# Kernel optimization log

Measured on AMD Instinct MI355X. Metric: run time of the kernel, lower is better.

## Reference

```python
import jax, jax.numpy as jnp
import numpy as np

EPSILON = 1e-05


def setup_inputs() -> dict:
    key = jax.random.key(0)
    k1, k2, k3 = jax.random.split(key, 3)
    B, T, D, K = 8, 4096, 256, 2048
    hidden_states = jax.random.normal(k1, (B, T, D), dtype=jnp.float32)
    embed_sum = jax.random.normal(k2, (K, D), dtype=jnp.float32)
    # cluster usage counts are positive in practice
    cluster_usage = jax.random.uniform(k3, (K,), dtype=jnp.float32) * 10.0 + 0.1
    return {
        "hidden_states": hidden_states,
        "embed_sum": embed_sum,
        "cluster_usage": cluster_usage,
    }


def reference(hidden_states, embed_sum, cluster_usage):
    # embed = embed_sum / clamp(cluster_usage, eps)   -> [K, D]
    embed = embed_sum / jnp.clip(cluster_usage, EPSILON, None)[:, None]

    shape = hidden_states.shape
    x = hidden_states.reshape(-1, shape[-1])  # [N, D]

    # squared L2 distances via norm expansion (argmin equals argmin of cdist p=2)
    x_sq = jnp.sum(x * x, axis=-1, keepdims=True)          # [N, 1]
    e_sq = jnp.sum(embed * embed, axis=-1)[None, :]         # [1, K]
    dots = jnp.einsum("nd,kd->nk", x, embed)               # [N, K]
    dists = x_sq - 2.0 * dots + e_sq                        # [N, K]

    embed_ind = jnp.argmin(dists, axis=-1)                 # [N]
    embed_ind = embed_ind.reshape(shape[:-1])              # [B, T]

    # decode: embedding lookup
    quantize = embed[embed_ind]                             # [B, T, D]
    return quantize, embed_ind
```

## Files before the change

kernel.cpp:

```cpp
#include <hip/hip_runtime.h>
#include <float.h>
#include <stdint.h>


#define EPSILON 1e-5f
#define DELTA   1e-3f

constexpr int D     = 256;
constexpr int K_TOT = 2048;

constexpr int RES_H      = 32768;
constexpr int ESQ_H      = 65536;
constexpr int LDS_HALVES = 69632;
constexpr int DYN_LDS    = LDS_HALVES * 2;

typedef _Float16 half8v  __attribute__((ext_vector_type(8)));
typedef _Float16 half4v  __attribute__((ext_vector_type(4)));
typedef float    f32x4   __attribute__((ext_vector_type(4)));

#define GLL(SRC, DST)                                                   \
  __builtin_amdgcn_global_load_lds(                                     \
      (const __attribute__((address_space(1))) void*)(SRC),             \
      (__attribute__((address_space(3))) void*)(DST), 16, 0, 0)

__global__ void prep_kernel(const float* __restrict__ es,
                            const float* __restrict__ usage,
                            _Float16* __restrict__ ec,
                            float* __restrict__ esq,
                            int* __restrict__ counter) {
  const int bx   = blockIdx.x;
  const int t    = threadIdx.x;
  const int wid  = t >> 6;
  const int lane = t & 63;
  if (bx < K_TOT / 4) {
    const int k = bx * 4 + wid;
    const float u = fmaxf(usage[k], EPSILON);
    const float4 v = *(const float4*)(es + (size_t)k * D + lane * 4);
    float4 e;
    e.x = v.x / u; e.y = v.y / u; e.z = v.z / u; e.w = v.w / u;
    half4v h, lo;
    h.x = (_Float16)e.x; lo.x = (_Float16)(e.x - (float)h.x);
    h.y = (_Float16)e.y; lo.y = (_Float16)(e.y - (float)h.y);
    h.z = (_Float16)e.z; lo.z = (_Float16)(e.z - (float)h.z);
    h.w = (_Float16)e.w; lo.w = (_Float16)(e.w - (float)h.w);
    *(half4v*)(ec + (size_t)k * 512 + lane * 4)       = h;
    *(half4v*)(ec + (size_t)k * 512 + 256 + lane * 4) = lo;
    float s = e.x * e.x + e.y * e.y + e.z * e.z + e.w * e.w;
    #pragma unroll
    for (int m = 1; m < 64; m <<= 1) s += __shfl_xor(s, m, 64);
    if (lane == 0) esq[k] = s;
  } else {
    if (t == 0) *counter = 0;
  }
}

__global__ __launch_bounds__(512, 2)
void mm_kernel(const float* __restrict__ x, const _Float16* __restrict__ ec,
               const float* __restrict__ esq, const float* __restrict__ es,
               const float* __restrict__ usage,
               float* __restrict__ out_q, float* __restrict__ out_i,
               int* __restrict__ list, int* __restrict__ counter,
               unsigned long long* __restrict__ rmin,
               int* __restrict__ tick, int N) {
  extern __shared__ __align__(16) _Float16 lds[];
  const int t    = threadIdx.x;
  const int lane = t & 63;
  const int q    = lane >> 4;
  const int l15  = lane & 15;
  const int wid  = t >> 6;
  const int wn   = wid >> 1;
  const int wk   = wid & 1;
  const int n0   = blockIdx.x * 128;

  float* esq_lds = (float*)&lds[ESQ_H];
  {
    const float4 ev = *(const float4*)(esq + t * 4);
    *(float4*)&esq_lds[t * 4] = ev;
  }

  const int prow  = t >> 2;
  const int pc    = t & 3;
  const int wbase = (t >> 6) * 512 + ((t & 63) ^ ((t >> 3) & 3)) * 8;
  #pragma unroll
  for (int i = 0; i < 8; ++i) {
    const float* src = x + (size_t)(n0 + prow) * D + i * 32 + pc * 8;
    const float4 f0 = *(const float4*)src;
    const float4 f1 = *(const float4*)(src + 4);
    const float f[8] = {f0.x, f0.y, f0.z, f0.w, f1.x, f1.y, f1.z, f1.w};
    half8v hv, lv;
    #pragma unroll
    for (int e = 0; e < 8; ++e) {
      const _Float16 h = (_Float16)f[e];
      hv[e] = h;
      lv[e] = (_Float16)(f[e] - (float)h);
    }
    *(half8v*)&lds[i * 4096 + wbase]         = hv;
    *(half8v*)&lds[RES_H + i * 4096 + wbase] = lv;
  }
  __syncthreads();

  const int gA = l15 * 4 + q;
  const int sp = (gA ^ ((l15 >> 1) & 3)) * 8;

  half8v ahr[8][2];
  #pragma unroll
  for (int s = 0; s < 8; ++s)
    #pragma unroll
    for (int mi = 0; mi < 2; ++mi)
      ahr[s][mi] = *(const half8v*)&lds[s * 4096 + wn * 1024 + mi * 512 + sp];
  __syncthreads();

  const int r0 = t >> 3;
  const int cl = (t & 7) ^ (r0 & 7);
  const _Float16* pB = ec + (size_t)r0 * 512 + cl * 8;

  #pragma unroll
  for (int s = 0; s < 2; ++s) {
    const _Float16* sp0 = pB + s * 64;
    GLL(sp0,         &lds[s * 8192 + t * 8]);
    GLL(sp0 + 32768, &lds[s * 8192 + 4096 + t * 8]);
  }

  int bfoff[4][2];
  #pragma unroll
  for (int ni = 0; ni < 4; ++ni)
    #pragma unroll
    for (int j = 0; j < 2; ++j)
      bfoff[ni][j] = (wk * 64 + ni * 16 + l15) * 64 +
                     (((j << 2) + q) ^ (l15 & 7)) * 8;

  float rd0[2][4], rd1[2][4];
  int   ri0[2][4];
  #pragma unroll
  for (int mi = 0; mi < 2; ++mi)
    #pragma unroll
    for (int r = 0; r < 4; ++r) {
      rd0[mi][r] = FLT_MAX; rd1[mi][r] = FLT_MAX; ri0[mi][r] = 0x7fffffff;
    }

  for (int kt = 0; kt < 16; ++kt) {
    int   kc[4];
    float eqv[4];
    #pragma unroll
    for (int ni = 0; ni < 4; ++ni) {
      kc[ni]  = kt * 128 + wk * 64 + ni * 16 + l15;
      eqv[ni] = esq_lds[kc[ni]];
    }

    f32x4 acc[2][4] = {};

    #pragma unroll
    for (int hv2 = 0; hv2 < 4; ++hv2) {
      const int ivl = kt * 4 + hv2;
      asm volatile("s_waitcnt vmcnt(0)" ::: "memory");
      __builtin_amdgcn_s_barrier();
      __builtin_amdgcn_sched_barrier(0);

      if (ivl < 63) {
        #pragma unroll
        for (int u = 0; u < 2; ++u) {
          const int ns = ivl * 2 + 2 + u;
          const _Float16* np = pB + (size_t)(ns >> 3) * 65536 + (ns & 7) * 64;
          const int nb = (ns & 3) * 8192;
          GLL(np,         &lds[nb + t * 8]);
          GLL(np + 32768, &lds[nb + 4096 + t * 8]);
        }
      }

      __builtin_amdgcn_s_setprio(1);
      #pragma unroll
      for (int u = 0; u < 2; ++u) {
        const int sidx = hv2 * 2 + u;
        const int ss   = kt * 8 + sidx;
        const int bb   = (ss & 3) * 8192;
        #pragma unroll
        for (int j = 0; j < 2; ++j) {
          half8v bf[4];
          #pragma unroll
          for (int ni = 0; ni < 4; ++ni)
            bf[ni] = *(const half8v*)&lds[bb + bfoff[ni][j]];
          const int ks = (sidx & 3) * 2 + j;
          if (sidx < 4) {
            half8v al[2];
            #pragma unroll
            for (int mi = 0; mi < 2; ++mi)
              al[mi] = *(const half8v*)
                  &lds[RES_H + ks * 4096 + wn * 1024 + mi * 512 + sp];
            #pragma unroll
            for (int mi = 0; mi < 2; ++mi)
              #pragma unroll
              for (int ni = 0; ni < 4; ++ni)
                acc[mi][ni] = __builtin_amdgcn_mfma_f32_16x16x32_f16(
                    ahr[ks][mi], bf[ni], acc[mi][ni], 0, 0, 0);
            #pragma unroll
            for (int mi = 0; mi < 2; ++mi)
              #pragma unroll
              for (int ni = 0; ni < 4; ++ni)
                acc[mi][ni] = __builtin_amdgcn_mfma_f32_16x16x32_f16(
                    al[mi], bf[ni], acc[mi][ni], 0, 0, 0);
          } else {
            #pragma unroll
            for (int mi = 0; mi < 2; ++mi)
              #pragma unroll
              for (int ni = 0; ni < 4; ++ni)
                acc[mi][ni] = __builtin_amdgcn_mfma_f32_16x16x32_f16(
                    ahr[ks][mi], bf[ni], acc[mi][ni], 0, 0, 0);
          }
        }
      }
      __builtin_amdgcn_s_setprio(0);
    }

    #pragma unroll
    for (int ni = 0; ni < 4; ++ni) {
      #pragma unroll
      for (int mi = 0; mi < 2; ++mi) {
        #pragma unroll
        for (int r = 0; r < 4; ++r) {
          const float d = fmaf(-2.f, acc[mi][ni][r], eqv[ni]);
          if (d < rd0[mi][r]) {
            rd1[mi][r] = rd0[mi][r]; rd0[mi][r] = d; ri0[mi][r] = kc[ni];
          } else {
            rd1[mi][r] = fminf(rd1[mi][r], d);
          }
        }
      }
    }
  }
  __syncthreads();

  float* ex = (float*)lds;
  #pragma unroll
  for (int mi = 0; mi < 2; ++mi) {
    #pragma unroll
    for (int r = 0; r < 4; ++r) {
      float d0 = rd0[mi][r], d1 = rd1[mi][r];
      int   i0 = ri0[mi][r];
      #pragma unroll
      for (int off = 1; off < 16; off <<= 1) {
        const float od0 = __shfl_xor(d0, off, 16);
        const int   oi0 = __shfl_xor(i0, off, 16);
        const float od1 = __shfl_xor(d1, off, 16);
        if (od0 < d0 || (od0 == d0 && oi0 < i0)) {
          d1 = fminf(d0, od1); d0 = od0; i0 = oi0;
        } else {
          d1 = fminf(d1, od0);
        }
      }
      if (l15 == mi * 8 + r) {
        const int row = wn * 32 + mi * 16 + q * 4 + r;
        *(float4*)&ex[(row * 2 + wk) * 4] =
            make_float4(d0, __int_as_float(i0), d1, 0.f);
      }
    }
  }
  __syncthreads();

  {
    const int row = t >> 2;
    const int seg = t & 3;
    const float4 a = *(const float4*)&ex[(row * 2 + 0) * 4];
    const float4 b = *(const float4*)&ex[(row * 2 + 1) * 4];
    float d0, d1; int i0;
    const int ia = __float_as_int(a.y), ib = __float_as_int(b.y);
    if (b.x < a.x || (b.x == a.x && ib < ia)) {
      d0 = b.x; i0 = ib; d1 = fminf(a.x, b.z);
    } else {
      d0 = a.x; i0 = ia; d1 = fminf(a.z, b.x);
    }
    const int n = n0 + row;
    const float u  = fmaxf(usage[i0], EPSILON);
    const float4* src = (const float4*)(es + (size_t)i0 * D);
    float4*       dst = (float4*)(out_q + (size_t)n * D);
    #pragma unroll
    for (int i = 0; i < 16; ++i) {
      const int j = i * 4 + seg;
      const float4 e = src[j];
      dst[j] = make_float4(e.x / u, e.y / u, e.z / u, e.w / u);
    }
    if (seg == 0) {
      out_i[n] = (float)i0;
      if (d1 - d0 < DELTA) {
        rmin[n] = 0xFFFFFFFFFFFFFFFFull;
        tick[n] = 0;
        const int pos = atomicAdd(counter, 1);
        list[pos] = n;
      }
    }
  }
}

__global__ void repair_kernel(const float* __restrict__ x,
                              const float* __restrict__ es,
                              const float* __restrict__ usage,
                              const float* __restrict__ esq,
                              const int* __restrict__ list,
                              const int* __restrict__ counter,
                              unsigned long long* __restrict__ rmin,
                              int* __restrict__ tick,
                              float* __restrict__ out_q,
                              float* __restrict__ out_i) {
  __shared__ float xs[256];
  const int t    = threadIdx.x;
  const int w    = t >> 6;
  const int lane = t & 63;
  const int cnt  = *counter;
  const int kseg = blockIdx.x & 7;

  for (int j = blockIdx.x >> 3; j < cnt; j += 256) {
    const int n = list[j];
    __syncthreads();
    xs[t] = x[(size_t)n * D + t];
    __syncthreads();
    const float4 xv = *(const float4*)&xs[lane * 4];

    float bd = FLT_MAX;
    int   bi = 0x7fffffff;
    const int kb0 = kseg * 256 + w * 64;
    for (int kk = 0; kk < 64; kk += 4) {
      const int kbase = kb0 + kk;
      float pd[4];
      #pragma unroll
      for (int j2 = 0; j2 < 4; ++j2) {
        const int k = kbase + j2;
        const float rs = 1.0f / fmaxf(usage[k], EPSILON);
        const float4 e = *(const float4*)(es + (size_t)k * D + lane * 4);
        float p = xv.x * (e.x * rs);
        p = fmaf(xv.y, e.y * rs, p);
        p = fmaf(xv.z, e.z * rs, p);
        pd[j2] = fmaf(xv.w, e.w * rs, p);
      }
      #pragma unroll
      for (int off = 1; off < 64; off <<= 1) {
        pd[0] += __shfl_xor(pd[0], off, 64);
        pd[1] += __shfl_xor(pd[1], off, 64);
        pd[2] += __shfl_xor(pd[2], off, 64);
        pd[3] += __shfl_xor(pd[3], off, 64);
      }
      #pragma unroll
      for (int j2 = 0; j2 < 4; ++j2) {
        const float dst = fmaf(-2.f, pd[j2], esq[kbase + j2]);
        if (dst < bd) { bd = dst; bi = kbase + j2; }
      }
    }
    int widx = -1;
    if (lane == 0) {
      uint32_t ub = __float_as_uint(bd);
      ub = (ub & 0x80000000u) ? ~ub : (ub | 0x80000000u);
      const unsigned long long pk =
          ((unsigned long long)ub << 32) | (unsigned)bi;
      atomicMin(&rmin[n], pk);
      __threadfence();
      const int done = atomicAdd(&tick[n], 1);
      if (done == 31) {
        __threadfence();
        const unsigned long long fin = atomicAdd(&rmin[n], 0ull);
        widx = (int)(fin & 0x7fffffffu);
      }
    }
    widx = __shfl(widx, 0, 64);
    if (widx >= 0) {
      const float u = fmaxf(usage[widx], EPSILON);
      const float4 e = *(const float4*)(es + (size_t)widx * D + lane * 4);
      *(float4*)(out_q + (size_t)n * D + lane * 4) =
          make_float4(e.x / u, e.y / u, e.z / u, e.w / u);
      if (lane == 0) out_i[n] = (float)widx;
    }
  }
}

constexpr int TN = 128;
constexpr int DC = 32;
constexpr int KS = 2;
constexpr int RS = 196;

__global__ void esq_kernel(const float* __restrict__ es,
                           const float* __restrict__ usage,
                           float* __restrict__ esq) {
  const int lane = threadIdx.x & 63;
  const int w    = threadIdx.x >> 6;
  const int k    = blockIdx.x * 4 + w;
  const float u  = fmaxf(usage[k], EPSILON);
  const float4 e = *(const float4*)(es + (size_t)k * D + lane * 4);
  const float a = e.x / u, b = e.y / u, c = e.z / u, d = e.w / u;
  float s = a * a + b * b + c * c + d * d;
  #pragma unroll
  for (int m = 1; m < 64; m <<= 1) s += __shfl_xor(s, m, 64);
  if (lane == 0) esq[k] = s;
}

__global__ __launch_bounds__(256, 2)
void dist_kernel(const float* __restrict__ x,
                 const float* __restrict__ es,
                 const float* __restrict__ usage,
                 const float* __restrict__ esq,
                 float* __restrict__ bestd,
                 int* __restrict__ besti, int N) {
  __shared__ float smX[DC * RS];
  __shared__ float smE[DC * RS];
  const int t    = threadIdx.x;
  const int tx   = t & 15;
  const int ty   = t >> 4;
  const int n0   = blockIdx.x * TN;
  const int half = blockIdx.y;

  float best[8];
  int   bidx[8];
  #pragma unroll
  for (int i = 0; i < 8; ++i) { best[i] = FLT_MAX; bidx[i] = 0; }

  for (int kt = 0; kt < (K_TOT / KS) / 128; ++kt) {
    const int k0 = half * (K_TOT / KS) + kt * 128;
    float acc[8][8];
    #pragma unroll
    for (int i = 0; i < 8; ++i)
      #pragma unroll
      for (int j = 0; j < 8; ++j) acc[i][j] = 0.f;

    for (int dc = 0; dc < D; dc += DC) {
      __syncthreads();
      #pragma unroll
      for (int i = 0; i < 4; ++i) {
        const int f    = i * 256 + t;
        const int row  = f >> 3;
        const int c4   = f & 7;
        const int pcol = row + ((row >> 3) << 2);
        const float4 xv =
            *(const float4*)(x + (size_t)(n0 + row) * D + dc + c4 * 4);
        smX[(c4 * 4 + 0) * RS + pcol] = xv.x;
        smX[(c4 * 4 + 1) * RS + pcol] = xv.y;
        smX[(c4 * 4 + 2) * RS + pcol] = xv.z;
        smX[(c4 * 4 + 3) * RS + pcol] = xv.w;
        const int kk = k0 + row;
        const float rs = 1.0f / fmaxf(usage[kk], EPSILON);
        const float4 ev =
            *(const float4*)(es + (size_t)kk * D + dc + c4 * 4);
        smE[(c4 * 4 + 0) * RS + pcol] = ev.x * rs;
        smE[(c4 * 4 + 1) * RS + pcol] = ev.y * rs;
        smE[(c4 * 4 + 2) * RS + pcol] = ev.z * rs;
        smE[(c4 * 4 + 3) * RS + pcol] = ev.w * rs;
      }
      __syncthreads();
      #pragma unroll 4
      for (int d = 0; d < DC; ++d) {
        const float* px = &smX[d * RS + ty * 12];
        const float* pe = &smE[d * RS + tx * 12];
        const float4 xa = *(const float4*)px;
        const float4 xb = *(const float4*)(px + 4);
        const float4 ea = *(const float4*)pe;
        const float4 eb = *(const float4*)(pe + 4);
        const float xr[8] = {xa.x, xa.y, xa.z, xa.w, xb.x, xb.y, xb.z, xb.w};
        const float er[8] = {ea.x, ea.y, ea.z, ea.w, eb.x, eb.y, eb.z, eb.w};
        #pragma unroll
        for (int i = 0; i < 8; ++i)
          #pragma unroll
          for (int jj = 0; jj < 8; ++jj)
            acc[i][jj] = fmaf(xr[i], er[jj], acc[i][jj]);
      }
    }
    #pragma unroll
    for (int jj = 0; jj < 8; ++jj) {
      const int k = k0 + tx * 8 + jj;
      const float eq = esq[k];
      #pragma unroll
      for (int i = 0; i < 8; ++i) {
        const float dst = fmaf(-2.0f, acc[i][jj], eq);
        if (dst < best[i]) { best[i] = dst; bidx[i] = k; }
      }
    }
  }
  __syncthreads();
  float* rd = smX;
  int*   ri = (int*)smE;
  #pragma unroll
  for (int i = 0; i < 8; ++i) {
    const int r = ty * 8 + i;
    rd[tx * TN + r] = best[i];
    ri[tx * TN + r] = bidx[i];
  }
  __syncthreads();
  for (int off = 8; off >= 1; off >>= 1) {
    if (tx < off) {
      #pragma unroll
      for (int i = 0; i < 8; ++i) {
        const int r = ty * 8 + i;
        const float da = rd[tx * TN + r], db = rd[(tx + off) * TN + r];
        const int   ia = ri[tx * TN + r], ib = ri[(tx + off) * TN + r];
        if (db < da || (db == da && ib < ia)) {
          rd[tx * TN + r] = db;
          ri[tx * TN + r] = ib;
        }
      }
    }
    __syncthreads();
  }
  if (tx == 0) {
    #pragma unroll
    for (int i = 0; i < 8; ++i) {
      const int r = ty * 8 + i;
      bestd[(size_t)half * N + n0 + r] = rd[r];
      besti[(size_t)half * N + n0 + r] = ri[r];
    }
  }
}

__global__ void gather_kernel(const float* __restrict__ es,
                              const float* __restrict__ usage,
                              const float* __restrict__ bestd,
                              const int* __restrict__ besti,
                              float* __restrict__ out_q,
                              float* __restrict__ out_i, int N) {
  const int w    = threadIdx.x >> 6;
  const int lane = threadIdx.x & 63;
  const int n    = blockIdx.x * 4 + w;
  const float d0 = bestd[n];
  const float d1 = bestd[(size_t)N + n];
  const int   i0 = besti[n];
  const int   i1 = besti[(size_t)N + n];
  const int idx = (d1 < d0) ? i1 : i0;
  const float u = fmaxf(usage[idx], EPSILON);
  const float4 e = *(const float4*)(es + (size_t)idx * D + lane * 4);
  float4 qv;
  qv.x = e.x / u; qv.y = e.y / u; qv.z = e.z / u; qv.w = e.w / u;
  *(float4*)(out_q + (size_t)n * D + lane * 4) = qv;
  if (lane == 0) out_i[n] = (float)idx;
}

extern "C" void kernel_launch(void* const* d_in, const int* in_sizes, int n_in,
                              void* d_out, int out_size, void* d_ws, size_t ws_size,
                              hipStream_t stream) {
  const float* x     = (const float*)d_in[0];
  const float* es    = (const float*)d_in[1];
  const float* usage = (const float*)d_in[2];
  const int N = in_sizes[0] / D;

  float* out_q = (float*)d_out;
  float* out_i = out_q + (size_t)N * D;

  const size_t EB = (size_t)K_TOT * 512 * 2;
  const size_t off_esq  = EB;
  const size_t off_list = off_esq + 8192;
  const size_t off_cnt  = off_list + (size_t)N * 4;
  const size_t off_rmin = off_cnt + 16;
  const size_t off_tick = off_rmin + (size_t)N * 8;
  const size_t NEED     = off_tick + (size_t)N * 4;

  char* wsb = (char*)d_ws;

  hipError_t attr_ok = hipFuncSetAttribute(
      (const void*)mm_kernel, hipFuncAttributeMaxDynamicSharedMemorySize,
      DYN_LDS);

  if (ws_size >= NEED && attr_ok == hipSuccess && (N % 128) == 0) {
    _Float16* ec   = (_Float16*)wsb;
    float*    esq  = (float*)(wsb + off_esq);
    int*      list = (int*)(wsb + off_list);
    int*      cnt  = (int*)(wsb + off_cnt);
    unsigned long long* rmin = (unsigned long long*)(wsb + off_rmin);
    int*      tick = (int*)(wsb + off_tick);

    prep_kernel<<<K_TOT / 4 + 1, 256, 0, stream>>>(es, usage, ec, esq, cnt);
    mm_kernel<<<N / 128, 512, DYN_LDS, stream>>>(x, ec, esq, es, usage,
                                                 out_q, out_i, list, cnt,
                                                 rmin, tick, N);
    repair_kernel<<<2048, 256, 0, stream>>>(x, es, usage, esq, list, cnt,
                                            rmin, tick, out_q, out_i);
  } else {
    float* ws    = (float*)d_ws;
    float* esq   = ws;
    float* bestd = ws + K_TOT;
    int*   besti = (int*)(ws + K_TOT + (size_t)KS * N);
    esq_kernel<<<K_TOT / 4, 256, 0, stream>>>(es, usage, esq);
    dist_kernel<<<dim3(N / TN, KS), 256, 0, stream>>>(x, es, usage, esq,
                                                      bestd, besti, N);
    gather_kernel<<<N / 4, 256, 0, stream>>>(es, usage, bestd, besti,
                                             out_q, out_i, N);
  }
}
```

Before: 196.8 us.

## Cache scaled codebook slice in LDS for repair kernel

The repair kernel now has each block own a fixed 32-code slice of the codebook. It pre-scales that slice by the inverse usage and keeps it in shared memory, so the slice is read once per block instead of once per flagged row. The grid decomposition changes from 8 K-segments with 256 row strides to 64 K-segments with 32 row strides. The per-row minimum is now reduced across the four waves in LDS before a single atomic, and the completion tick threshold is updated to 64. The block uses 32KB of static LDS and adds extra block-wide barriers per row, and the row-level parallelism inside each K-segment is smaller.

```diff
diff --git a/kernel.cpp b/kernel.cpp
--- a/kernel.cpp
+++ b/kernel.cpp
@@ -290,82 +290,105 @@
   }
 }
 
-__global__ void repair_kernel(const float* __restrict__ x,
-                              const float* __restrict__ es,
-                              const float* __restrict__ usage,
-                              const float* __restrict__ esq,
-                              const int* __restrict__ list,
-                              const int* __restrict__ counter,
-                              unsigned long long* __restrict__ rmin,
-                              int* __restrict__ tick,
-                              float* __restrict__ out_q,
-                              float* __restrict__ out_i) {
+__global__ __launch_bounds__(256)
+void repair_kernel(const float* __restrict__ x,
+                   const float* __restrict__ es,
+                   const float* __restrict__ usage,
+                   const float* __restrict__ esq,
+                   const int* __restrict__ list,
+                   const int* __restrict__ counter,
+                   unsigned long long* __restrict__ rmin,
+                   int* __restrict__ tick,
+                   float* __restrict__ out_q,
+                   float* __restrict__ out_i) {
+  __shared__ float esl[32 * 256];
+  __shared__ float eql[32];
   __shared__ float xs[256];
+  __shared__ float bwd[4];
+  __shared__ int   bwi[4];
+  __shared__ int   bcast;
   const int t    = threadIdx.x;
   const int w    = t >> 6;
   const int lane = t & 63;
+  const int kseg = blockIdx.x & 63;
+  const int rstr = blockIdx.x >> 6;
+  const int k0   = kseg * 32;
   const int cnt  = *counter;
-  const int kseg = blockIdx.x & 7;
-
-  for (int j = blockIdx.x >> 3; j < cnt; j += 256) {
+
+  #pragma unroll
+  for (int i = 0; i < 8; ++i) {
+    const int idx = i * 256 + t;
+    const int kk  = idx >> 6;
+    const int c4  = idx & 63;
+    const float rs = 1.0f / fmaxf(usage[k0 + kk], EPSILON);
+    const float4 e = *(const float4*)(es + (size_t)(k0 + kk) * D + c4 * 4);
+    *(float4*)&esl[kk * 256 + c4 * 4] =
+        make_float4(e.x * rs, e.y * rs, e.z * rs, e.w * rs);
+  }
+  if (t < 32) eql[t] = esq[k0 + t];
+  __syncthreads();
+
+  for (int j = rstr; j < cnt; j += 32) {
     const int n = list[j];
-    __syncthreads();
     xs[t] = x[(size_t)n * D + t];
     __syncthreads();
     const float4 xv = *(const float4*)&xs[lane * 4];
 
+    float pd[8];
+    #pragma unroll
+    for (int kk8 = 0; kk8 < 8; ++kk8) {
+      const float4 e = *(const float4*)&esl[(w * 8 + kk8) * 256 + lane * 4];
+      float p = xv.x * e.x;
+      p = fmaf(xv.y, e.y, p);
+      p = fmaf(xv.z, e.z, p);
+      pd[kk8] = fmaf(xv.w, e.w, p);
+    }
+    #pragma unroll
+    for (int off = 1; off < 64; off <<= 1) {
+      #pragma unroll
+      for (int kk8 = 0; kk8 < 8; ++kk8)
+        pd[kk8] += __shfl_xor(pd[kk8], off, 64);
+    }
     float bd = FLT_MAX;
     int   bi = 0x7fffffff;
-    const int kb0 = kseg * 256 + w * 64;
-    for (int kk = 0; kk < 64; kk += 4) {
-      const int kbase = kb0 + kk;
-      float pd[4];
-      #pragma unroll
-      for (int j2 = 0; j2 < 4; ++j2) {
-        const int k = kbase + j2;
-        const float rs = 1.0f / fmaxf(usage[k], EPSILON);
-        const float4 e = *(const float4*)(es + (size_t)k * D + lane * 4);
-        float p = xv.x * (e.x * rs);
-        p = fmaf(xv.y, e.y * rs, p);
-        p = fmaf(xv.z, e.z * rs, p);
-        pd[j2] = fmaf(xv.w, e.w * rs, p);
-      }
-      #pragma unroll
-      for (int off = 1; off < 64; off <<= 1) {
-        pd[0] += __shfl_xor(pd[0], off, 64);
-        pd[1] += __shfl_xor(pd[1], off, 64);
-        pd[2] += __shfl_xor(pd[2], off, 64);
-        pd[3] += __shfl_xor(pd[3], off, 64);
-      }
-      #pragma unroll
-      for (int j2 = 0; j2 < 4; ++j2) {
-        const float dst = fmaf(-2.f, pd[j2], esq[kbase + j2]);
-        if (dst < bd) { bd = dst; bi = kbase + j2; }
-      }
-    }
-    int widx = -1;
-    if (lane == 0) {
-      uint32_t ub = __float_as_uint(bd);
+    #pragma unroll
+    for (int kk8 = 0; kk8 < 8; ++kk8) {
+      const float dst = fmaf(-2.f, pd[kk8], eql[w * 8 + kk8]);
+      if (dst < bd) { bd = dst; bi = k0 + w * 8 + kk8; }
+    }
+    if (lane == 0) { bwd[w] = bd; bwi[w] = bi; }
+    __syncthreads();
+
+    if (t == 0) {
+      float d = bwd[0]; int i0 = bwi[0];
+      #pragma unroll
+      for (int ww = 1; ww < 4; ++ww)
+        if (bwd[ww] < d || (bwd[ww] == d && bwi[ww] < i0)) {
+          d = bwd[ww]; i0 = bwi[ww];
+        }
+      uint32_t ub = __float_as_uint(d);
       ub = (ub & 0x80000000u) ? ~ub : (ub | 0x80000000u);
       const unsigned long long pk =
-          ((unsigned long long)ub << 32) | (unsigned)bi;
+          ((unsigned long long)ub << 32) | (unsigned)i0;
       atomicMin(&rmin[n], pk);
       __threadfence();
       const int done = atomicAdd(&tick[n], 1);
-      if (done == 31) {
+      int widx = -1;
+      if (done == 63) {
         __threadfence();
         const unsigned long long fin = atomicAdd(&rmin[n], 0ull);
         widx = (int)(fin & 0x7fffffffu);
       }
-    }
-    widx = __shfl(widx, 0, 64);
+      bcast = widx;
+    }
+    __syncthreads();
+    const int widx = bcast;
     if (widx >= 0) {
       const float u = fmaxf(usage[widx], EPSILON);
-      const float4 e = *(const float4*)(es + (size_t)widx * D + lane * 4);
-      *(float4*)(out_q + (size_t)n * D + lane * 4) =
-          make_float4(e.x / u, e.y / u, e.z / u, e.w / u);
-      if (lane == 0) out_i[n] = (float)widx;
-    }
+      out_q[(size_t)n * D + t] = es[(size_t)widx * D + t] / u;
+      if (t == 0) out_i[n] = (float)widx;
+    }
+    __syncthreads();
   }
 }
 
```

Result: slower. 202.1 us (+2.7%).
